# Kernel tuning notes

Hardware: AMD Instinct MI355X
Metric: run time of the kernel (lower is better)

## Reference

```python
import jax, jax.numpy as jnp
import numpy as np

N_USER = 50000
N_ITEM = 100000
EMB = 64
NNZ = 1200000
BATCH = 4096
RATE = 0.1          # node_dropout[0]
N_LAYERS = 4        # len(layer_size); make_hop needs >=4 hops for 5 prefix means
N_NODES = N_USER + N_ITEM


def setup_inputs() -> dict:
    key = jax.random.key(0)
    ks = jax.random.split(key, 12)
    return {
        "user_emb": jax.random.normal(ks[0], (N_USER, EMB), dtype=jnp.float32) * 0.1,
        "item_emb": jax.random.normal(ks[1], (N_ITEM, EMB), dtype=jnp.float32) * 0.1,
        "adj_vals": jax.random.uniform(ks[2], (NNZ,), dtype=jnp.float32),
        "drop_u": jax.random.uniform(ks[3], (NNZ,), dtype=jnp.float32),
        "adj_rows": jax.random.randint(ks[4], (NNZ,), 0, N_NODES, dtype=jnp.int32),
        "adj_cols": jax.random.randint(ks[5], (NNZ,), 0, N_NODES, dtype=jnp.int32),
        "users": jax.random.randint(ks[6], (BATCH,), 0, N_USER, dtype=jnp.int32),
        "pos_items": jax.random.randint(ks[7], (BATCH,), 0, N_ITEM, dtype=jnp.int32),
        "neg_items": jax.random.randint(ks[8], (BATCH,), 0, N_ITEM, dtype=jnp.int32),
        "u_a": jax.random.randint(ks[9], (BATCH,), 0, 5, dtype=jnp.int32),
        "p_a": jax.random.randint(ks[10], (BATCH,), 0, 5, dtype=jnp.int32),
        "n_a": jax.random.randint(ks[11], (BATCH,), 0, 5, dtype=jnp.int32),
        "index": 0,
    }


def _make_hop(user_emb, item_emb, adj_vals, drop_u, adj_rows, adj_cols):
    # sparse dropout: floor(1 - rate + u) gives a 0/1 keep mask; rescale by 1/(1-rate).
    mask = jnp.floor((1.0 - RATE) + drop_u)
    vals = adj_vals * mask * (1.0 / (1.0 - RATE))
    ego = jnp.concatenate([user_emb, item_emb], axis=0)  # [N, d]
    all_embs = [ego]
    for _ in range(N_LAYERS):
        # SpMM: out[r] = sum_e vals[e] * ego[cols[e]] for rows[e] == r
        msgs = vals[:, None] * ego[adj_cols]             # [nnz, d]
        ego = jax.ops.segment_sum(msgs, adj_rows, num_segments=N_NODES)
        all_embs.append(ego)
    # prefix means over hops 0..i
    result = [all_embs[0]]
    running = all_embs[0]
    for i in range(1, 5):
        running = running + all_embs[i]
        result.append(running / float(i + 1))
    return jnp.stack(result)  # [5, N, d]


def reference(user_emb, item_emb, adj_vals, drop_u, adj_rows, adj_cols,
              users, pos_items, neg_items, u_a, p_a, n_a, index):
    embed = _make_hop(user_emb, item_emb, adj_vals, drop_u, adj_rows, adj_cols)
    n_user = user_emb.shape[0]
    if index == 0:
        u = embed[u_a, users]
        p = embed[p_a, pos_items + n_user]
        n = embed[n_a, neg_items + n_user]
    else:
        u = embed[u_a, users + n_user]
        p = embed[p_a, pos_items]
        n = embed[n_a, neg_items]
    return (u, p, n)
```

## Files before the change

### kernel.cpp

```cpp
#include <hip/hip_runtime.h>
#include <stdint.h>

#define N_USER_C  50000
#define N_ITEM_C  100000
#define N_NODES_C 150000
#define EMB_C     64
#define NNZ_C     1200000
#define BATCH_C   4096

#define BKT_SHIFT 9
#define BKT_ROWS  (1 << BKT_SHIFT)
#define NB        ((N_NODES_C + BKT_ROWS - 1) / BKT_ROWS)
#define CH        8192
#define NBLK      ((NNZ_C + CH - 1) / CH)
#define N2        (NB * NBLK)
#define COL_MASK  0x3FFFF

typedef _Float16 h16;
typedef _Float16 h16x4 __attribute__((ext_vector_type(4)));

__global__ __launch_bounds__(1024) void k_bin_count(const float* __restrict__ du,
                                                    const int* __restrict__ rows,
                                                    int* __restrict__ cnt2) {
    __shared__ int bk[NB];
    int t = threadIdx.x, blk = blockIdx.x;
    for (int i = t; i < NB; i += 1024) bk[i] = 0;
    __syncthreads();
    int base = blk * CH;
    for (int i = 0; i < CH; i += 1024) {
        int e = base + i + t;
        if (e < NNZ_C && floorf(0.9f + du[e]) != 0.0f)
            atomicAdd(&bk[rows[e] >> BKT_SHIFT], 1);
    }
    __syncthreads();
    for (int i = t; i < NB; i += 1024) cnt2[i * NBLK + blk] = bk[i];
}

__global__ __launch_bounds__(256) void k_btot(const int* __restrict__ cnt2,
                                              int* __restrict__ btot) {
    __shared__ int red[256];
    int t = threadIdx.x, i = blockIdx.x;
    red[t] = (t < NBLK) ? cnt2[i * NBLK + t] : 0;
    __syncthreads();
    for (int off = 128; off > 0; off >>= 1) {
        if (t < off) red[t] += red[t + off];
        __syncthreads();
    }
    if (t == 0) btot[i] = red[0];
}

__global__ __launch_bounds__(512) void k_bbase(const int* __restrict__ btot,
                                               int* __restrict__ bbase,
                                               int* __restrict__ base2,
                                               int* __restrict__ row_start) {
    __shared__ int sh[512];
    int t = threadIdx.x;
    int v0 = (t < NB) ? btot[t] : 0;
    sh[t] = v0;
    __syncthreads();
    for (int off = 1; off < 512; off <<= 1) {
        int v = (t >= off) ? sh[t - off] : 0;
        __syncthreads();
        sh[t] += v;
        __syncthreads();
    }
    if (t < NB) bbase[t] = sh[t] - v0;
    if (t == 511) {
        base2[N2] = sh[511];
        row_start[N_NODES_C] = sh[511];
    }
}

__global__ __launch_bounds__(256) void k_bscan(const int* __restrict__ cnt2,
                                               const int* __restrict__ bbase,
                                               int* __restrict__ base2) {
    __shared__ int sh[256];
    int t = threadIdx.x, i = blockIdx.x;
    int v0 = (t < NBLK) ? cnt2[i * NBLK + t] : 0;
    sh[t] = v0;
    __syncthreads();
    for (int off = 1; off < 256; off <<= 1) {
        int v = (t >= off) ? sh[t - off] : 0;
        __syncthreads();
        sh[t] += v;
        __syncthreads();
    }
    if (t < NBLK) base2[i * NBLK + t] = bbase[i] + sh[t] - v0;
}

__global__ __launch_bounds__(1024) void k_bin_write(const float* __restrict__ av,
                                                    const float* __restrict__ du,
                                                    const int* __restrict__ rows,
                                                    const int* __restrict__ cols,
                                                    const int* __restrict__ base2,
                                                    int2* __restrict__ ev) {
    __shared__ int cur[NB];
    int t = threadIdx.x, blk = blockIdx.x;
    for (int i = t; i < NB; i += 1024) cur[i] = base2[i * NBLK + blk];
    __syncthreads();
    int base = blk * CH;
    for (int i = 0; i < CH; i += 1024) {
        int e = base + i + t;
        if (e < NNZ_C) {
            float m = floorf(0.9f + du[e]);
            if (m != 0.0f) {
                float v = av[e] * m * (float)(1.0 / 0.9);
                int r = rows[e];
                int pos = atomicAdd(&cur[r >> BKT_SHIFT], 1);
                int2 p;
                p.x = ((r & (BKT_ROWS - 1)) << 18) | cols[e];
                p.y = __float_as_int(v);
                ev[pos] = p;
            }
        }
    }
}

__global__ __launch_bounds__(256) void k_bucket_sort(const int2* __restrict__ ev,
                                                     const int* __restrict__ base2,
                                                     int2* __restrict__ ep,
                                                     int* __restrict__ row_start) {
    __shared__ int rowcnt[BKT_ROWS];
    __shared__ int cursor[BKT_ROWS];
    __shared__ int tsum[256];
    int t = threadIdx.x, k = blockIdx.x;
    int rowBase = k << BKT_SHIFT;
    int bstart = base2[k * NBLK];
    int bend   = base2[(k + 1) * NBLK];
    for (int i = t; i < BKT_ROWS; i += 256) rowcnt[i] = 0;
    __syncthreads();
    for (int e = bstart + t; e < bend; e += 256)
        atomicAdd(&rowcnt[((unsigned)ev[e].x) >> 18], 1);
    __syncthreads();
    int a = rowcnt[2 * t], b = rowcnt[2 * t + 1];
    tsum[t] = a + b;
    __syncthreads();
    for (int off = 1; off < 256; off <<= 1) {
        int v = (t >= off) ? tsum[t - off] : 0;
        __syncthreads();
        tsum[t] += v;
        __syncthreads();
    }
    int excl = tsum[t] - (a + b);
    cursor[2 * t]     = excl;
    cursor[2 * t + 1] = excl + a;
    int gr = rowBase + 2 * t;
    if (gr < N_NODES_C)     row_start[gr]     = bstart + excl;
    if (gr + 1 < N_NODES_C) row_start[gr + 1] = bstart + excl + a;
    __syncthreads();
    for (int e = bstart + t; e < bend; e += 256) {
        int2 p = ev[e];
        int rl = ((unsigned)p.x) >> 18;
        int slot = atomicAdd(&cursor[rl], 1);
        p.x &= COL_MASK;
        ep[bstart + slot] = p;
    }
}

__global__ __launch_bounds__(256) void k_tohalf(const float4* __restrict__ ue,
                                                const float4* __restrict__ ie,
                                                h16x4* __restrict__ dst) {
    const int totalU = N_USER_C * EMB_C / 4;
    const int total  = N_NODES_C * EMB_C / 4;
    int stride = gridDim.x * blockDim.x;
    for (int i = blockIdx.x * blockDim.x + threadIdx.x; i < total; i += stride) {
        float4 v = (i < totalU) ? ue[i] : ie[i - totalU];
        h16x4 h;
        h[0] = (h16)v.x; h[1] = (h16)v.y; h[2] = (h16)v.z; h[3] = (h16)v.w;
        dst[i] = h;
    }
}

__global__ __launch_bounds__(256) void k_spmm_h(const int* __restrict__ rs,
                                                const int2* __restrict__ ep,
                                                const h16x4* __restrict__ ego,
                                                h16x4* __restrict__ nxt,
                                                const int* __restrict__ flag) {
    int wid  = (blockIdx.x * blockDim.x + threadIdx.x) >> 6;
    int lane = threadIdx.x & 63;
    if (wid >= N_NODES_C) return;
    if (flag && flag[wid] == 0) return;
    int start = rs[wid];
    int end   = rs[wid + 1];
    int eo = lane >> 4;
    int l  = lane & 15;
    float4 acc = make_float4(0.f, 0.f, 0.f, 0.f);
    #pragma unroll 2
    for (int it = start + eo; it < end; it += 4) {
        int2 p = ep[it];
        float v = __int_as_float(p.y);
        h16x4 g = ego[(int64_t)p.x * 16 + l];
        acc.x += v * (float)g[0]; acc.y += v * (float)g[1];
        acc.z += v * (float)g[2]; acc.w += v * (float)g[3];
    }
    acc.x += __shfl_xor(acc.x, 16); acc.y += __shfl_xor(acc.y, 16);
    acc.z += __shfl_xor(acc.z, 16); acc.w += __shfl_xor(acc.w, 16);
    acc.x += __shfl_xor(acc.x, 32); acc.y += __shfl_xor(acc.y, 32);
    acc.z += __shfl_xor(acc.z, 32); acc.w += __shfl_xor(acc.w, 32);
    if (lane < 16) {
        h16x4 h;
        h[0] = (h16)acc.x; h[1] = (h16)acc.y; h[2] = (h16)acc.z; h[3] = (h16)acc.w;
        nxt[(int64_t)wid * 16 + l] = h;
    }
}

__global__ __launch_bounds__(256) void k_flags(const int* __restrict__ rs,
                                               const int2* __restrict__ ep,
                                               int* __restrict__ flag3,
                                               int* __restrict__ flag2,
                                               const int* __restrict__ users,
                                               const int* __restrict__ pos,
                                               const int* __restrict__ neg,
                                               const int* __restrict__ ua,
                                               const int* __restrict__ pa,
                                               const int* __restrict__ na,
                                               const int* __restrict__ indexp) {
    int wid  = (blockIdx.x * blockDim.x + threadIdx.x) >> 6;
    int lane = threadIdx.x & 63;
    if (wid >= 3 * BATCH_C) return;
    int s = wid >> 12;
    int j = wid & (BATCH_C - 1);
    int a = (s == 0) ? ua[j] : (s == 1) ? pa[j] : na[j];
    if (a < 2) return;
    int idx0 = indexp[0];
    int row;
    if (s == 0)      row = users[j] + (idx0 ? N_USER_C : 0);
    else if (s == 1) row = pos[j]   + (idx0 ? 0 : N_USER_C);
    else             row = neg[j]   + (idx0 ? 0 : N_USER_C);
    if (lane == 0) {
        flag2[row] = 1;
        if (a >= 3) flag3[row] = 1;
    }
    if (a == 4) {
        int start = rs[row], end = rs[row + 1];
        for (int e = start + lane; e < end; e += 64)
            flag3[ep[e].x] = 1;
    }
}

__global__ __launch_bounds__(256) void k_flags2(const int* __restrict__ rs,
                                                const int2* __restrict__ ep,
                                                const int* __restrict__ flag3,
                                                int* __restrict__ flag2) {
    int wid  = (blockIdx.x * blockDim.x + threadIdx.x) >> 6;
    int lane = threadIdx.x & 63;
    if (wid >= N_NODES_C) return;
    if (flag3[wid] == 0) return;
    int start = rs[wid], end = rs[wid + 1];
    for (int e = start + lane; e < end; e += 64)
        flag2[ep[e].x] = 1;
}

__global__ __launch_bounds__(256) void k_spmm_g4(const int* __restrict__ rs,
                                                 const int2* __restrict__ ep,
                                                 const h16x4* __restrict__ ego,
                                                 float* __restrict__ out,
                                                 const int* __restrict__ users,
                                                 const int* __restrict__ pos,
                                                 const int* __restrict__ neg,
                                                 const int* __restrict__ ua,
                                                 const int* __restrict__ pa,
                                                 const int* __restrict__ na,
                                                 const int* __restrict__ indexp) {
    int wid  = (blockIdx.x * blockDim.x + threadIdx.x) >> 6;
    int lane = threadIdx.x & 63;
    if (wid >= 3 * BATCH_C) return;
    int s = wid >> 12;
    int j = wid & (BATCH_C - 1);
    int a = (s == 0) ? ua[j] : (s == 1) ? pa[j] : na[j];
    if (a != 4) return;
    int idx0 = indexp[0];
    int row;
    if (s == 0)      row = users[j] + (idx0 ? N_USER_C : 0);
    else if (s == 1) row = pos[j]   + (idx0 ? 0 : N_USER_C);
    else             row = neg[j]   + (idx0 ? 0 : N_USER_C);
    int start = rs[row];
    int end   = rs[row + 1];
    int eo = lane >> 4;
    int l  = lane & 15;
    float4 acc = make_float4(0.f, 0.f, 0.f, 0.f);
    for (int it = start + eo; it < end; it += 4) {
        int2 p = ep[it];
        float v = __int_as_float(p.y);
        h16x4 g = ego[(int64_t)p.x * 16 + l];
        acc.x += v * (float)g[0]; acc.y += v * (float)g[1];
        acc.z += v * (float)g[2]; acc.w += v * (float)g[3];
    }
    acc.x += __shfl_xor(acc.x, 16); acc.y += __shfl_xor(acc.y, 16);
    acc.z += __shfl_xor(acc.z, 16); acc.w += __shfl_xor(acc.w, 16);
    acc.x += __shfl_xor(acc.x, 32); acc.y += __shfl_xor(acc.y, 32);
    acc.z += __shfl_xor(acc.z, 32); acc.w += __shfl_xor(acc.w, 32);
    if (lane < 16) {
        float4* o = (float4*)out + (int64_t)wid * 16 + l;
        float4 cv = *o;
        cv.x += acc.x; cv.y += acc.y; cv.z += acc.z; cv.w += acc.w;
        *o = cv;
    }
}

__global__ __launch_bounds__(256) void k_gather(const float* __restrict__ srcU,
                                                const float* __restrict__ srcI,
                                                int pivot,
                                                float* __restrict__ out,
                                                const int* __restrict__ users,
                                                const int* __restrict__ pos,
                                                const int* __restrict__ neg,
                                                const int* __restrict__ ua,
                                                const int* __restrict__ pa,
                                                const int* __restrict__ na,
                                                const int* __restrict__ indexp) {
    int t = blockIdx.x * blockDim.x + threadIdx.x;
    if (t >= 3 * BATCH_C * EMB_C) return;
    int d = t & 63;
    int b = t >> 6;
    int s = b >> 12;
    int j = b & (BATCH_C - 1);
    int idx0 = indexp[0];
    int row;
    if (s == 0)      row = users[j] + (idx0 ? N_USER_C : 0);
    else if (s == 1) row = pos[j]   + (idx0 ? 0 : N_USER_C);
    else             row = neg[j]   + (idx0 ? 0 : N_USER_C);
    const float* sp = (row < pivot) ? (srcU + (int64_t)row * EMB_C)
                                    : (srcI + (int64_t)(row - pivot) * EMB_C);
    out[t] = sp[d];
}

__global__ __launch_bounds__(256) void k_gather_h(const h16* __restrict__ src,
                                                  float* __restrict__ out,
                                                  const int* __restrict__ users,
                                                  const int* __restrict__ pos,
                                                  const int* __restrict__ neg,
                                                  const int* __restrict__ ua,
                                                  const int* __restrict__ pa,
                                                  const int* __restrict__ na,
                                                  const int* __restrict__ indexp,
                                                  int hop) {
    int t = blockIdx.x * blockDim.x + threadIdx.x;
    if (t >= 3 * BATCH_C * EMB_C) return;
    int d = t & 63;
    int b = t >> 6;
    int s = b >> 12;
    int j = b & (BATCH_C - 1);
    int idx0 = indexp[0];
    int row, a;
    if (s == 0)      { row = users[j] + (idx0 ? N_USER_C : 0); a = ua[j]; }
    else if (s == 1) { row = pos[j]   + (idx0 ? 0 : N_USER_C); a = pa[j]; }
    else             { row = neg[j]   + (idx0 ? 0 : N_USER_C); a = na[j]; }
    if (hop <= a)
        out[t] += (float)src[(int64_t)row * EMB_C + d];
}

__global__ __launch_bounds__(256) void k_scale(float* __restrict__ out,
                                               const int* __restrict__ ua,
                                               const int* __restrict__ pa,
                                               const int* __restrict__ na) {
    int t = blockIdx.x * blockDim.x + threadIdx.x;
    if (t >= 3 * BATCH_C * EMB_C) return;
    int b = t >> 6;
    int s = b >> 12;
    int j = b & (BATCH_C - 1);
    int a = (s == 0) ? ua[j] : (s == 1) ? pa[j] : na[j];
    out[t] /= (float)(a + 1);
}

extern "C" void kernel_launch(void* const* d_in, const int* in_sizes, int n_in,
                              void* d_out, int out_size, void* d_ws, size_t ws_size,
                              hipStream_t stream) {
    const float* user_emb = (const float*)d_in[0];
    const float* item_emb = (const float*)d_in[1];
    const float* adj_vals = (const float*)d_in[2];
    const float* drop_u   = (const float*)d_in[3];
    const int*   adj_rows = (const int*)d_in[4];
    const int*   adj_cols = (const int*)d_in[5];
    const int*   users    = (const int*)d_in[6];
    const int*   pos_it   = (const int*)d_in[7];
    const int*   neg_it   = (const int*)d_in[8];
    const int*   u_a      = (const int*)d_in[9];
    const int*   p_a      = (const int*)d_in[10];
    const int*   n_a      = (const int*)d_in[11];
    const int*   indexp   = (const int*)d_in[12];
    float* out = (float*)d_out;

    const size_t egoElems = (size_t)N_NODES_C * EMB_C;
    h16*   egoH0     = (h16*)d_ws;
    h16*   bufA      = egoH0 + egoElems;
    h16*   bufB      = bufA + egoElems;
    int2*  ep        = (int2*)(bufB + egoElems);
    int2*  ev        = ep + NNZ_C;
    int*   row_start = (int*)(ev + NNZ_C);
    int*   cnt2      = row_start + N_NODES_C + 1;
    int*   base2     = cnt2 + N2 + 1;
    int*   btot      = base2 + N2 + 1;
    int*   bbase     = btot + NB + 1;
    int*   flags3    = bbase + NB + 1;
    int*   flags2    = flags3 + N_NODES_C;

    k_bin_count<<<NBLK, 1024, 0, stream>>>(drop_u, adj_rows, cnt2);
    k_btot<<<NB, 256, 0, stream>>>(cnt2, btot);
    k_bbase<<<1, 512, 0, stream>>>(btot, bbase, base2, row_start);
    k_bscan<<<NB, 256, 0, stream>>>(cnt2, bbase, base2);
    k_bin_write<<<NBLK, 1024, 0, stream>>>(adj_vals, drop_u, adj_rows, adj_cols,
                                           base2, ev);
    k_bucket_sort<<<NB, 256, 0, stream>>>(ev, base2, ep, row_start);

    hipMemsetAsync(flags3, 0, 2 * N_NODES_C * sizeof(int), stream);
    k_flags<<<(3 * BATCH_C * 64 + 255) / 256, 256, 0, stream>>>(
        row_start, ep, flags3, flags2, users, pos_it, neg_it, u_a, p_a, n_a, indexp);
    k_flags2<<<(N_NODES_C * 64 + 255) / 256, 256, 0, stream>>>(
        row_start, ep, flags3, flags2);

    k_tohalf<<<2048, 256, 0, stream>>>((const float4*)user_emb,
                                       (const float4*)item_emb, (h16x4*)egoH0);
    const int GT = 3 * BATCH_C * EMB_C;
    k_gather<<<(GT + 255) / 256, 256, 0, stream>>>(user_emb, item_emb, N_USER_C, out,
                                                   users, pos_it, neg_it,
                                                   u_a, p_a, n_a, indexp);

    const int SPMM_BLOCKS = (N_NODES_C * 64 + 255) / 256;
    k_spmm_h<<<SPMM_BLOCKS, 256, 0, stream>>>(row_start, ep, (const h16x4*)egoH0,
                                              (h16x4*)bufA, (const int*)nullptr);
    k_gather_h<<<(GT + 255) / 256, 256, 0, stream>>>(bufA, out, users, pos_it, neg_it,
                                                     u_a, p_a, n_a, indexp, 1);
    k_spmm_h<<<SPMM_BLOCKS, 256, 0, stream>>>(row_start, ep, (const h16x4*)bufA,
                                              (h16x4*)bufB, flags2);
    k_gather_h<<<(GT + 255) / 256, 256, 0, stream>>>(bufB, out, users, pos_it, neg_it,
                                                     u_a, p_a, n_a, indexp, 2);
    k_spmm_h<<<SPMM_BLOCKS, 256, 0, stream>>>(row_start, ep, (const h16x4*)bufB,
                                              (h16x4*)bufA, flags3);
    k_gather_h<<<(GT + 255) / 256, 256, 0, stream>>>(bufA, out, users, pos_it, neg_it,
                                                     u_a, p_a, n_a, indexp, 3);
    k_spmm_g4<<<(3 * BATCH_C * 64 + 255) / 256, 256, 0, stream>>>(
        row_start, ep, (const h16x4*)bufA, out,
        users, pos_it, neg_it, u_a, p_a, n_a, indexp);

    k_scale<<<(GT + 255) / 256, 256, 0, stream>>>(out, u_a, p_a, n_a);
}
```

Baseline: 211.2 us.

## Fuse flag, gather and SpMM kernels to cut launch count

Merges independent kernels by splitting each grid into block ranges. The flag-building passes now share launches with the hop-1 SpMM, and the per-hop gathers share launches with the following SpMM. The memset moves into the bin-count kernel, the bucket-total reduction moves into the single-block scan, and the final scale is folded into each gather as a per-sample 1/(a+1) factor. The aim is to remove about ten launches and their serialization gaps, at the cost of a serial per-thread sum over NBLK entries in the single-block scan.

```diff
diff --git a/kernel.cpp b/kernel.cpp
--- a/kernel.cpp
+++ b/kernel.cpp
@@ -16,14 +16,20 @@
 #define N2        (NB * NBLK)
 #define COL_MASK  0x3FFFF
 
+#define SPMM_B    37500
+#define GB        3072
+#define THB       2048
+
 typedef _Float16 h16;
 typedef _Float16 h16x4 __attribute__((ext_vector_type(4)));
 
 __global__ __launch_bounds__(1024) void k_bin_count(const float* __restrict__ du,
                                                     const int* __restrict__ rows,
-                                                    int* __restrict__ cnt2) {
+                                                    int* __restrict__ cnt2,
+                                                    int* __restrict__ flagz) {
     __shared__ int bk[NB];
     int t = threadIdx.x, blk = blockIdx.x;
+    for (int i = blk * 1024 + t; i < 2 * N_NODES_C; i += NBLK * 1024) flagz[i] = 0;
     for (int i = t; i < NB; i += 1024) bk[i] = 0;
     __syncthreads();
     int base = blk * CH;
@@ -36,27 +42,18 @@
     for (int i = t; i < NB; i += 1024) cnt2[i * NBLK + blk] = bk[i];
 }
 
-__global__ __launch_bounds__(256) void k_btot(const int* __restrict__ cnt2,
-                                              int* __restrict__ btot) {
-    __shared__ int red[256];
-    int t = threadIdx.x, i = blockIdx.x;
-    red[t] = (t < NBLK) ? cnt2[i * NBLK + t] : 0;
-    __syncthreads();
-    for (int off = 128; off > 0; off >>= 1) {
-        if (t < off) red[t] += red[t + off];
-        __syncthreads();
-    }
-    if (t == 0) btot[i] = red[0];
-}
-
-__global__ __launch_bounds__(512) void k_bbase(const int* __restrict__ btot,
+__global__ __launch_bounds__(512) void k_bbase(const int* __restrict__ cnt2,
                                                int* __restrict__ bbase,
                                                int* __restrict__ base2,
                                                int* __restrict__ row_start) {
     __shared__ int sh[512];
     int t = threadIdx.x;
-    int v0 = (t < NB) ? btot[t] : 0;
-    sh[t] = v0;
+    int s = 0;
+    if (t < NB) {
+        const int* p = cnt2 + t * NBLK;
+        for (int i = 0; i < NBLK; ++i) s += p[i];
+    }
+    sh[t] = s;
     __syncthreads();
     for (int off = 1; off < 512; off <<= 1) {
         int v = (t >= off) ? sh[t - off] : 0;
@@ -64,7 +61,7 @@
         sh[t] += v;
         __syncthreads();
     }
-    if (t < NB) bbase[t] = sh[t] - v0;
+    if (t < NB) bbase[t] = sh[t] - s;
     if (t == 511) {
         base2[N2] = sh[511];
         row_start[N_NODES_C] = sh[511];
@@ -157,27 +154,27 @@
     }
 }
 
-__global__ __launch_bounds__(256) void k_tohalf(const float4* __restrict__ ue,
-                                                const float4* __restrict__ ie,
-                                                h16x4* __restrict__ dst) {
-    const int totalU = N_USER_C * EMB_C / 4;
-    const int total  = N_NODES_C * EMB_C / 4;
-    int stride = gridDim.x * blockDim.x;
-    for (int i = blockIdx.x * blockDim.x + threadIdx.x; i < total; i += stride) {
-        float4 v = (i < totalU) ? ue[i] : ie[i - totalU];
-        h16x4 h;
-        h[0] = (h16)v.x; h[1] = (h16)v.y; h[2] = (h16)v.z; h[3] = (h16)v.w;
-        dst[i] = h;
-    }
-}
-
-__global__ __launch_bounds__(256) void k_spmm_h(const int* __restrict__ rs,
-                                                const int2* __restrict__ ep,
-                                                const h16x4* __restrict__ ego,
-                                                h16x4* __restrict__ nxt,
-                                                const int* __restrict__ flag) {
-    int wid  = (blockIdx.x * blockDim.x + threadIdx.x) >> 6;
-    int lane = threadIdx.x & 63;
+__device__ __forceinline__ void batch_row_a(int wid, int idx0,
+                                            const int* __restrict__ users,
+                                            const int* __restrict__ pos,
+                                            const int* __restrict__ neg,
+                                            const int* __restrict__ ua,
+                                            const int* __restrict__ pa,
+                                            const int* __restrict__ na,
+                                            int& row, int& a) {
+    int s = wid >> 12;
+    int j = wid & (BATCH_C - 1);
+    if (s == 0)      { row = users[j] + (idx0 ? N_USER_C : 0); a = ua[j]; }
+    else if (s == 1) { row = pos[j]   + (idx0 ? 0 : N_USER_C); a = pa[j]; }
+    else             { row = neg[j]   + (idx0 ? 0 : N_USER_C); a = na[j]; }
+}
+
+__device__ __forceinline__ void spmm_row_body(int wid, int lane,
+                                              const int* __restrict__ rs,
+                                              const int2* __restrict__ ep,
+                                              const h16x4* __restrict__ ego,
+                                              h16x4* __restrict__ nxt,
+                                              const int* __restrict__ flag) {
     if (wid >= N_NODES_C) return;
     if (flag && flag[wid] == 0) return;
     int start = rs[wid];
@@ -204,56 +201,135 @@
     }
 }
 
-__global__ __launch_bounds__(256) void k_flags(const int* __restrict__ rs,
+__device__ __forceinline__ void gather_body(const h16* __restrict__ src,
+                                            float* __restrict__ out, int t, int hop,
+                                            int idx0,
+                                            const int* __restrict__ users,
+                                            const int* __restrict__ pos,
+                                            const int* __restrict__ neg,
+                                            const int* __restrict__ ua,
+                                            const int* __restrict__ pa,
+                                            const int* __restrict__ na) {
+    int d = t & 63;
+    int b = t >> 6;
+    int row, a;
+    batch_row_a(b, idx0, users, pos, neg, ua, pa, na, row, a);
+    if (hop <= a)
+        out[t] += (float)src[(int64_t)row * EMB_C + d] / (float)(a + 1);
+}
+
+__global__ __launch_bounds__(256) void k_prep(const float* __restrict__ ue,
+                                              const float* __restrict__ ie,
+                                              h16x4* __restrict__ dst,
+                                              float* __restrict__ out,
+                                              const int* __restrict__ users,
+                                              const int* __restrict__ pos,
+                                              const int* __restrict__ neg,
+                                              const int* __restrict__ ua,
+                                              const int* __restrict__ pa,
+                                              const int* __restrict__ na,
+                                              const int* __restrict__ indexp) {
+    if (blockIdx.x < GB) {
+        int t = blockIdx.x * 256 + threadIdx.x;
+        int d = t & 63;
+        int b = t >> 6;
+        int row, a;
+        batch_row_a(b, indexp[0], users, pos, neg, ua, pa, na, row, a);
+        const float* sp = (row < N_USER_C) ? (ue + (int64_t)row * EMB_C)
+                                           : (ie + (int64_t)(row - N_USER_C) * EMB_C);
+        out[t] = sp[d] / (float)(a + 1);
+    } else {
+        const int totalU = N_USER_C * EMB_C / 4;
+        const int total  = N_NODES_C * EMB_C / 4;
+        const int stride = THB * 256;
+        const float4* uev = (const float4*)ue;
+        const float4* iev = (const float4*)ie;
+        for (int i = (blockIdx.x - GB) * 256 + threadIdx.x; i < total; i += stride) {
+            float4 v = (i < totalU) ? uev[i] : iev[i - totalU];
+            h16x4 h;
+            h[0] = (h16)v.x; h[1] = (h16)v.y; h[2] = (h16)v.z; h[3] = (h16)v.w;
+            dst[i] = h;
+        }
+    }
+}
+
+__global__ __launch_bounds__(256) void k_spmm1f(const int* __restrict__ rs,
+                                                const int2* __restrict__ ep,
+                                                const h16x4* __restrict__ ego,
+                                                h16x4* __restrict__ nxt,
+                                                int* __restrict__ flag3,
+                                                int* __restrict__ flag2,
+                                                const int* __restrict__ users,
+                                                const int* __restrict__ pos,
+                                                const int* __restrict__ neg,
+                                                const int* __restrict__ ua,
+                                                const int* __restrict__ pa,
+                                                const int* __restrict__ na,
+                                                const int* __restrict__ indexp) {
+    int lane = threadIdx.x & 63;
+    if (blockIdx.x < SPMM_B) {
+        int wid = (blockIdx.x * 256 + threadIdx.x) >> 6;
+        spmm_row_body(wid, lane, rs, ep, ego, nxt, (const int*)nullptr);
+    } else {
+        int wid = ((blockIdx.x - SPMM_B) * 256 + threadIdx.x) >> 6;
+        if (wid >= 3 * BATCH_C) return;
+        int row, a;
+        batch_row_a(wid, indexp[0], users, pos, neg, ua, pa, na, row, a);
+        if (a < 2) return;
+        if (lane == 0) {
+            flag2[row] = 1;
+            if (a >= 3) flag3[row] = 1;
+        }
+        if (a == 4) {
+            int start = rs[row], end = rs[row + 1];
+            for (int e = start + lane; e < end; e += 64)
+                flag3[ep[e].x] = 1;
+        }
+    }
+}
+
+__global__ __launch_bounds__(256) void k_fg1(const int* __restrict__ rs,
+                                             const int2* __restrict__ ep,
+                                             const int* __restrict__ flag3,
+                                             int* __restrict__ flag2,
+                                             const h16* __restrict__ src,
+                                             float* __restrict__ out,
+                                             const int* __restrict__ users,
+                                             const int* __restrict__ pos,
+                                             const int* __restrict__ neg,
+                                             const int* __restrict__ ua,
+                                             const int* __restrict__ pa,
+                                             const int* __restrict__ na,
+                                             const int* __restrict__ indexp) {
+    if (blockIdx.x < SPMM_B) {
+        int wid  = (blockIdx.x * 256 + threadIdx.x) >> 6;
+        int lane = threadIdx.x & 63;
+        if (wid >= N_NODES_C || flag3[wid] == 0) return;
+        int start = rs[wid], end = rs[wid + 1];
+        for (int e = start + lane; e < end; e += 64)
+            flag2[ep[e].x] = 1;
+    } else {
+        int t = (blockIdx.x - SPMM_B) * 256 + threadIdx.x;
+        gather_body(src, out, t, 1, indexp[0], users, pos, neg, ua, pa, na);
+    }
+}
+
+__global__ __launch_bounds__(256) void k_spmm2(const int* __restrict__ rs,
                                                const int2* __restrict__ ep,
-                                               int* __restrict__ flag3,
-                                               int* __restrict__ flag2,
-                                               const int* __restrict__ users,
-                                               const int* __restrict__ pos,
-                                               const int* __restrict__ neg,
-                                               const int* __restrict__ ua,
-                                               const int* __restrict__ pa,
-                                               const int* __restrict__ na,
-                                               const int* __restrict__ indexp) {
-    int wid  = (blockIdx.x * blockDim.x + threadIdx.x) >> 6;
+                                               const h16x4* __restrict__ ego,
+                                               h16x4* __restrict__ nxt,
+                                               const int* __restrict__ flag) {
+    int wid  = (blockIdx.x * 256 + threadIdx.x) >> 6;
     int lane = threadIdx.x & 63;
-    if (wid >= 3 * BATCH_C) return;
-    int s = wid >> 12;
-    int j = wid & (BATCH_C - 1);
-    int a = (s == 0) ? ua[j] : (s == 1) ? pa[j] : na[j];
-    if (a < 2) return;
-    int idx0 = indexp[0];
-    int row;
-    if (s == 0)      row = users[j] + (idx0 ? N_USER_C : 0);
-    else if (s == 1) row = pos[j]   + (idx0 ? 0 : N_USER_C);
-    else             row = neg[j]   + (idx0 ? 0 : N_USER_C);
-    if (lane == 0) {
-        flag2[row] = 1;
-        if (a >= 3) flag3[row] = 1;
-    }
-    if (a == 4) {
-        int start = rs[row], end = rs[row + 1];
-        for (int e = start + lane; e < end; e += 64)
-            flag3[ep[e].x] = 1;
-    }
-}
-
-__global__ __launch_bounds__(256) void k_flags2(const int* __restrict__ rs,
-                                                const int2* __restrict__ ep,
-                                                const int* __restrict__ flag3,
-                                                int* __restrict__ flag2) {
-    int wid  = (blockIdx.x * blockDim.x + threadIdx.x) >> 6;
-    int lane = threadIdx.x & 63;
-    if (wid >= N_NODES_C) return;
-    if (flag3[wid] == 0) return;
-    int start = rs[wid], end = rs[wid + 1];
-    for (int e = start + lane; e < end; e += 64)
-        flag2[ep[e].x] = 1;
-}
-
-__global__ __launch_bounds__(256) void k_spmm_g4(const int* __restrict__ rs,
+    spmm_row_body(wid, lane, rs, ep, ego, nxt, flag);
+}
+
+__global__ __launch_bounds__(256) void k_spmm3g2(const int* __restrict__ rs,
                                                  const int2* __restrict__ ep,
                                                  const h16x4* __restrict__ ego,
+                                                 h16x4* __restrict__ nxt,
+                                                 const int* __restrict__ flag3,
+                                                 const h16* __restrict__ gsrc,
                                                  float* __restrict__ out,
                                                  const int* __restrict__ users,
                                                  const int* __restrict__ pos,
@@ -262,105 +338,62 @@
                                                  const int* __restrict__ pa,
                                                  const int* __restrict__ na,
                                                  const int* __restrict__ indexp) {
-    int wid  = (blockIdx.x * blockDim.x + threadIdx.x) >> 6;
-    int lane = threadIdx.x & 63;
+    if (blockIdx.x < SPMM_B) {
+        int wid  = (blockIdx.x * 256 + threadIdx.x) >> 6;
+        int lane = threadIdx.x & 63;
+        spmm_row_body(wid, lane, rs, ep, ego, nxt, flag3);
+    } else {
+        int t = (blockIdx.x - SPMM_B) * 256 + threadIdx.x;
+        gather_body(gsrc, out, t, 2, indexp[0], users, pos, neg, ua, pa, na);
+    }
+}
+
+__global__ __launch_bounds__(256) void k_g3g4(const int* __restrict__ rs,
+                                              const int2* __restrict__ ep,
+                                              const h16x4* __restrict__ ego,
+                                              float* __restrict__ out,
+                                              const int* __restrict__ users,
+                                              const int* __restrict__ pos,
+                                              const int* __restrict__ neg,
+                                              const int* __restrict__ ua,
+                                              const int* __restrict__ pa,
+                                              const int* __restrict__ na,
+                                              const int* __restrict__ indexp) {
+    int gid  = blockIdx.x * 256 + threadIdx.x;
+    int wid  = gid >> 6;
+    int lane = gid & 63;
     if (wid >= 3 * BATCH_C) return;
-    int s = wid >> 12;
-    int j = wid & (BATCH_C - 1);
-    int a = (s == 0) ? ua[j] : (s == 1) ? pa[j] : na[j];
-    if (a != 4) return;
-    int idx0 = indexp[0];
-    int row;
-    if (s == 0)      row = users[j] + (idx0 ? N_USER_C : 0);
-    else if (s == 1) row = pos[j]   + (idx0 ? 0 : N_USER_C);
-    else             row = neg[j]   + (idx0 ? 0 : N_USER_C);
-    int start = rs[row];
-    int end   = rs[row + 1];
-    int eo = lane >> 4;
-    int l  = lane & 15;
+    int row, a;
+    batch_row_a(wid, indexp[0], users, pos, neg, ua, pa, na, row, a);
+    if (a < 3) return;
     float4 acc = make_float4(0.f, 0.f, 0.f, 0.f);
-    for (int it = start + eo; it < end; it += 4) {
-        int2 p = ep[it];
-        float v = __int_as_float(p.y);
-        h16x4 g = ego[(int64_t)p.x * 16 + l];
-        acc.x += v * (float)g[0]; acc.y += v * (float)g[1];
-        acc.z += v * (float)g[2]; acc.w += v * (float)g[3];
-    }
-    acc.x += __shfl_xor(acc.x, 16); acc.y += __shfl_xor(acc.y, 16);
-    acc.z += __shfl_xor(acc.z, 16); acc.w += __shfl_xor(acc.w, 16);
-    acc.x += __shfl_xor(acc.x, 32); acc.y += __shfl_xor(acc.y, 32);
-    acc.z += __shfl_xor(acc.z, 32); acc.w += __shfl_xor(acc.w, 32);
+    if (a == 4) {
+        int start = rs[row], end = rs[row + 1];
+        int eo = lane >> 4;
+        int l  = lane & 15;
+        for (int it = start + eo; it < end; it += 4) {
+            int2 p = ep[it];
+            float v = __int_as_float(p.y);
+            h16x4 g = ego[(int64_t)p.x * 16 + l];
+            acc.x += v * (float)g[0]; acc.y += v * (float)g[1];
+            acc.z += v * (float)g[2]; acc.w += v * (float)g[3];
+        }
+        acc.x += __shfl_xor(acc.x, 16); acc.y += __shfl_xor(acc.y, 16);
+        acc.z += __shfl_xor(acc.z, 16); acc.w += __shfl_xor(acc.w, 16);
+        acc.x += __shfl_xor(acc.x, 32); acc.y += __shfl_xor(acc.y, 32);
+        acc.z += __shfl_xor(acc.z, 32); acc.w += __shfl_xor(acc.w, 32);
+    }
     if (lane < 16) {
-        float4* o = (float4*)out + (int64_t)wid * 16 + l;
+        h16x4 g = ego[(int64_t)row * 16 + lane];
+        float inv = 1.0f / (float)(a + 1);
+        float4* o = (float4*)out + (int64_t)wid * 16 + lane;
         float4 cv = *o;
-        cv.x += acc.x; cv.y += acc.y; cv.z += acc.z; cv.w += acc.w;
+        cv.x += ((float)g[0] + acc.x) * inv;
+        cv.y += ((float)g[1] + acc.y) * inv;
+        cv.z += ((float)g[2] + acc.z) * inv;
+        cv.w += ((float)g[3] + acc.w) * inv;
         *o = cv;
     }
-}
-
-__global__ __launch_bounds__(256) void k_gather(const float* __restrict__ srcU,
-                                                const float* __restrict__ srcI,
-                                                int pivot,
-                                                float* __restrict__ out,
-                                                const int* __restrict__ users,
-                                                const int* __restrict__ pos,
-                                                const int* __restrict__ neg,
-                                                const int* __restrict__ ua,
-                                                const int* __restrict__ pa,
-                                                const int* __restrict__ na,
-                                                const int* __restrict__ indexp) {
-    int t = blockIdx.x * blockDim.x + threadIdx.x;
-    if (t >= 3 * BATCH_C * EMB_C) return;
-    int d = t & 63;
-    int b = t >> 6;
-    int s = b >> 12;
-    int j = b & (BATCH_C - 1);
-    int idx0 = indexp[0];
-    int row;
-    if (s == 0)      row = users[j] + (idx0 ? N_USER_C : 0);
-    else if (s == 1) row = pos[j]   + (idx0 ? 0 : N_USER_C);
-    else             row = neg[j]   + (idx0 ? 0 : N_USER_C);
-    const float* sp = (row < pivot) ? (srcU + (int64_t)row * EMB_C)
-                                    : (srcI + (int64_t)(row - pivot) * EMB_C);
-    out[t] = sp[d];
-}
-
-__global__ __launch_bounds__(256) void k_gather_h(const h16* __restrict__ src,
-                                                  float* __restrict__ out,
-                                                  const int* __restrict__ users,
-                                                  const int* __restrict__ pos,
-                                                  const int* __restrict__ neg,
-                                                  const int* __restrict__ ua,
-                                                  const int* __restrict__ pa,
-                                                  const int* __restrict__ na,
-                                                  const int* __restrict__ indexp,
-                                                  int hop) {
-    int t = blockIdx.x * blockDim.x + threadIdx.x;
-    if (t >= 3 * BATCH_C * EMB_C) return;
-    int d = t & 63;
-    int b = t >> 6;
-    int s = b >> 12;
-    int j = b & (BATCH_C - 1);
-    int idx0 = indexp[0];
-    int row, a;
-    if (s == 0)      { row = users[j] + (idx0 ? N_USER_C : 0); a = ua[j]; }
-    else if (s == 1) { row = pos[j]   + (idx0 ? 0 : N_USER_C); a = pa[j]; }
-    else             { row = neg[j]   + (idx0 ? 0 : N_USER_C); a = na[j]; }
-    if (hop <= a)
-        out[t] += (float)src[(int64_t)row * EMB_C + d];
-}
-
-__global__ __launch_bounds__(256) void k_scale(float* __restrict__ out,
-                                               const int* __restrict__ ua,
-                                               const int* __restrict__ pa,
-                                               const int* __restrict__ na) {
-    int t = blockIdx.x * blockDim.x + threadIdx.x;
-    if (t >= 3 * BATCH_C * EMB_C) return;
-    int b = t >> 6;
-    int s = b >> 12;
-    int j = b & (BATCH_C - 1);
-    int a = (s == 0) ? ua[j] : (s == 1) ? pa[j] : na[j];
-    out[t] /= (float)(a + 1);
 }
 
 extern "C" void kernel_launch(void* const* d_in, const int* in_sizes, int n_in,
@@ -390,48 +423,31 @@
     int*   row_start = (int*)(ev + NNZ_C);
     int*   cnt2      = row_start + N_NODES_C + 1;
     int*   base2     = cnt2 + N2 + 1;
-    int*   btot      = base2 + N2 + 1;
-    int*   bbase     = btot + NB + 1;
+    int*   bbase     = base2 + N2 + 1;
     int*   flags3    = bbase + NB + 1;
     int*   flags2    = flags3 + N_NODES_C;
 
-    k_bin_count<<<NBLK, 1024, 0, stream>>>(drop_u, adj_rows, cnt2);
-    k_btot<<<NB, 256, 0, stream>>>(cnt2, btot);
-    k_bbase<<<1, 512, 0, stream>>>(btot, bbase, base2, row_start);
+    k_bin_count<<<NBLK, 1024, 0, stream>>>(drop_u, adj_rows, cnt2, flags3);
+    k_bbase<<<1, 512, 0, stream>>>(cnt2, bbase, base2, row_start);
     k_bscan<<<NB, 256, 0, stream>>>(cnt2, bbase, base2);
     k_bin_write<<<NBLK, 1024, 0, stream>>>(adj_vals, drop_u, adj_rows, adj_cols,
                                            base2, ev);
     k_bucket_sort<<<NB, 256, 0, stream>>>(ev, base2, ep, row_start);
 
-    hipMemsetAsync(flags3, 0, 2 * N_NODES_C * sizeof(int), stream);
-    k_flags<<<(3 * BATCH_C * 64 + 255) / 256, 256, 0, stream>>>(
-        row_start, ep, flags3, flags2, users, pos_it, neg_it, u_a, p_a, n_a, indexp);
-    k_flags2<<<(N_NODES_C * 64 + 255) / 256, 256, 0, stream>>>(
-        row_start, ep, flags3, flags2);
-
-    k_tohalf<<<2048, 256, 0, stream>>>((const float4*)user_emb,
-                                       (const float4*)item_emb, (h16x4*)egoH0);
-    const int GT = 3 * BATCH_C * EMB_C;
-    k_gather<<<(GT + 255) / 256, 256, 0, stream>>>(user_emb, item_emb, N_USER_C, out,
-                                                   users, pos_it, neg_it,
-                                                   u_a, p_a, n_a, indexp);
-
-    const int SPMM_BLOCKS = (N_NODES_C * 64 + 255) / 256;
-    k_spmm_h<<<SPMM_BLOCKS, 256, 0, stream>>>(row_start, ep, (const h16x4*)egoH0,
-                                              (h16x4*)bufA, (const int*)nullptr);
-    k_gather_h<<<(GT + 255) / 256, 256, 0, stream>>>(bufA, out, users, pos_it, neg_it,
-                                                     u_a, p_a, n_a, indexp, 1);
-    k_spmm_h<<<SPMM_BLOCKS, 256, 0, stream>>>(row_start, ep, (const h16x4*)bufA,
-                                              (h16x4*)bufB, flags2);
-    k_gather_h<<<(GT + 255) / 256, 256, 0, stream>>>(bufB, out, users, pos_it, neg_it,
-                                                     u_a, p_a, n_a, indexp, 2);
-    k_spmm_h<<<SPMM_BLOCKS, 256, 0, stream>>>(row_start, ep, (const h16x4*)bufB,
-                                              (h16x4*)bufA, flags3);
-    k_gather_h<<<(GT + 255) / 256, 256, 0, stream>>>(bufA, out, users, pos_it, neg_it,
-                                                     u_a, p_a, n_a, indexp, 3);
-    k_spmm_g4<<<(3 * BATCH_C * 64 + 255) / 256, 256, 0, stream>>>(
-        row_start, ep, (const h16x4*)bufA, out,
-        users, pos_it, neg_it, u_a, p_a, n_a, indexp);
-
-    k_scale<<<(GT + 255) / 256, 256, 0, stream>>>(out, u_a, p_a, n_a);
-}
+    k_prep<<<GB + THB, 256, 0, stream>>>(user_emb, item_emb, (h16x4*)egoH0, out,
+                                         users, pos_it, neg_it, u_a, p_a, n_a, indexp);
+
+    k_spmm1f<<<SPMM_B + GB, 256, 0, stream>>>(row_start, ep, (const h16x4*)egoH0,
+                                              (h16x4*)bufA, flags3, flags2,
+                                              users, pos_it, neg_it, u_a, p_a, n_a, indexp);
+    k_fg1<<<SPMM_B + GB, 256, 0, stream>>>(row_start, ep, flags3, flags2,
+                                           bufA, out,
+                                           users, pos_it, neg_it, u_a, p_a, n_a, indexp);
+    k_spmm2<<<SPMM_B, 256, 0, stream>>>(row_start, ep, (const h16x4*)bufA,
+                                        (h16x4*)bufB, flags2);
+    k_spmm3g2<<<SPMM_B + GB, 256, 0, stream>>>(row_start, ep, (const h16x4*)bufB,
+                                               (h16x4*)bufA, flags3, bufB, out,
+                                               users, pos_it, neg_it, u_a, p_a, n_a, indexp);
+    k_g3g4<<<GB, 256, 0, stream>>>(row_start, ep, (const h16x4*)bufA, out,
+                                   users, pos_it, neg_it, u_a, p_a, n_a, indexp);
+}
```

Measured after the change: 194.1 us. 8.1% less time.
